# Kernel optimization log

Measured on AMD Instinct MI355X. Metric: run time of the kernel, lower is better.

The kernel has to match this reference:

```python
import jax, jax.numpy as jnp
import numpy as np

B, S, D = 2, 2048, 1024
NH, NKV = 16, 4
HD = D // NH
KVD = NKV * HD
NE, MM = 8, 4
INTER = MM * D // NE  # 512
ROPE_BASE = 10000.0
ALPHA, BETA, GATE, DT = 0.95, 0.3, 0.1, 0.1
MU_MIN, MU_MAX, VMAX = 0.5, 1.5, 3.0


def rms_norm(x):
    # torch F.rms_norm with eps=None -> finfo(dtype).eps, no learned weight
    return x * jax.lax.rsqrt(jnp.mean(x * x, axis=-1, keepdims=True) + jnp.finfo(x.dtype).eps)


def rope_tables(seq_len, dtype):
    inv_freq = 1.0 / ROPE_BASE ** (jnp.arange(0, HD, 2, dtype=jnp.float32) / HD)
    t = jnp.arange(seq_len, dtype=jnp.float32)
    freqs = jnp.outer(t, inv_freq)  # [S, HD/2]
    return jnp.cos(freqs).astype(dtype)[None, None], jnp.sin(freqs).astype(dtype)[None, None]


def apply_rotary(x, cos, sin):
    half = x.shape[-1] // 2
    x1, x2 = x[..., :half], x[..., half:]
    return jnp.concatenate((x1 * cos + x2 * sin, -x1 * sin + x2 * cos), axis=-1)


def attention(n, cq_w, ck_w, cv_w, proj_w, q_gain):
    q = jnp.einsum('bsd,od->bso', n, cq_w).reshape(B, S, NH, HD).transpose(0, 2, 1, 3)
    k = jnp.einsum('bsd,od->bso', n, ck_w).reshape(B, S, NKV, HD).transpose(0, 2, 1, 3)
    v = jnp.einsum('bsd,od->bso', n, cv_w).reshape(B, S, NKV, HD).transpose(0, 2, 1, 3)
    q, k = rms_norm(q), rms_norm(k)
    cos, sin = rope_tables(S, q.dtype)
    q, k = apply_rotary(q, cos, sin), apply_rotary(k, cos, sin)
    q = q * q_gain[None, :, None, None]
    rep = NH // NKV  # GQA: repeat kv heads
    k = jnp.repeat(k, rep, axis=1)
    v = jnp.repeat(v, rep, axis=1)
    scale = 1.0 / np.sqrt(HD).astype(np.float32)
    scores = jnp.einsum('bhqd,bhkd->bhqk', q, k) * scale
    causal = jnp.tril(jnp.ones((S, S), bool))
    scores = jnp.where(causal[None, None], scores, jnp.finfo(scores.dtype).min)
    probs = jax.nn.softmax(scores, axis=-1)
    y = jnp.einsum('bhqk,bhkd->bhqd', probs, v)
    y = y.transpose(0, 2, 1, 3).reshape(B, S, D)
    return jnp.einsum('bsd,od->bso', y, proj_w)


def moe(m, gate_up, down, eids):
    # faithful to TokenRoutedMLP: dense per-expert GEMM, masked accumulate
    flat = m.reshape(-1, D)
    fids = eids.reshape(-1)
    out = jnp.zeros_like(flat)
    for e in range(NE):
        gu = flat @ gate_up[e]                       # [T, 2*INTER]
        g, u = gu[:, :INTER], gu[:, INTER:]
        h = (jax.nn.silu(g) * u) @ down[e]           # [T, D]
        out = out + h * (fids == e)[:, None].astype(flat.dtype)
    return out.reshape(B, S, D)


def setup_inputs():
    key = jax.random.key(0)
    ks = jax.random.split(key, 10)
    w = lambda k, shape: jax.random.normal(k, shape, jnp.float32) * 0.02
    return {
        'x': jax.random.normal(ks[0], (B, S, D), jnp.float32),
        'x0': jax.random.normal(ks[1], (B, S, D), jnp.float32),
        'vel': jnp.zeros((B, S, D), jnp.float32),
        'resid_mix': jnp.stack((jnp.ones(D, jnp.float32), jnp.zeros(D, jnp.float32))),
        'attn_scale': jnp.ones(D, jnp.float32),
        'mlp_scale': jnp.ones(D, jnp.float32),
        'cq_w': w(ks[2], (D, D)),
        'ck_w': w(ks[3], (KVD, D)),
        'cv_w': w(ks[4], (KVD, D)),
        'proj_w': w(ks[5], (D, D)),
        'q_gain': jnp.ones(NH, jnp.float32),
        'mu': jnp.full((D,), 1.0, jnp.float32),
        'gate_up': w(ks[6], (NE, D, 2 * INTER)),
        'down': w(ks[7], (NE, INTER, D)),
        'eids': jax.random.randint(ks[8], (B, S), 0, NE),
    }


def reference(x, x0, vel, resid_mix, attn_scale, mlp_scale, cq_w, ck_w, cv_w, proj_w, q_gain, mu, gate_up, down, eids):
    x = resid_mix[0][None, None, :] * x + resid_mix[1][None, None, :] * x0
    n = rms_norm(x)
    x = x + attn_scale[None, None, :] * attention(n, cq_w, ck_w, cv_w, proj_w, q_gain)
    # PID dynamics
    mu_c = jnp.clip(mu, MU_MIN, MU_MAX)
    v_next = jnp.clip(ALPHA * vel - BETA * (x - mu_c[None, None, :]), -VMAX, VMAX)
    x = x + DT * GATE * v_next
    x = x + mlp_scale[None, None, :] * moe(rms_norm(x), gate_up, down, eids)
    return x, v_next
```

## Files before the change

### kernel.cpp

```cpp
#include <hip/hip_runtime.h>
#include <hip/hip_bf16.h>
#include <math.h>

#define NBATCH 2
#define NSEQ   2048
#define NDIM   1024
#define NHEAD  16
#define NKVH   4
#define HDIM   64
#define KVD    256
#define NEXP   8
#define NINTER 512
#define NTOK   (NBATCH*NSEQ)
#define QKVN   1536
#define MAXTILE 40
#define RMS_EPS 1.1920929e-07f
#define LN_10000 9.210340371976184f
#define QSCALE (0.125f * 1.44269504088896f)
#define DEFER_THR 11.5f

typedef __attribute__((ext_vector_type(8))) short bf16x8;
typedef __attribute__((ext_vector_type(4))) short short4v;
typedef __attribute__((ext_vector_type(4))) float f32x4;

__device__ __forceinline__ short f2b(float f) {
  return __builtin_bit_cast(short, (__bf16)f);
}
__device__ __forceinline__ float b2f(short s) {
  unsigned u = ((unsigned)(unsigned short)s) << 16;
  return __builtin_bit_cast(float, u);
}
__device__ __forceinline__ float ex2(float x) {
  float r; asm("v_exp_f32 %0, %1" : "=v"(r) : "v"(x)); return r;
}
__device__ __forceinline__ void load_lds16(const short* g, short* l) {
  __builtin_amdgcn_global_load_lds((const __attribute__((address_space(1))) void*)g,
                                   (__attribute__((address_space(3))) void*)l, 16, 0, 0);
}

__device__ __forceinline__ float wred64(float v) {
#pragma unroll
  for (int m = 32; m >= 1; m >>= 1) v += __shfl_xor(v, m);
  return v;
}

__global__ __launch_bounds__(256) void k_w_prep(
    const float* __restrict__ cq, const float* __restrict__ ck,
    const float* __restrict__ cv, const float* __restrict__ pw,
    const float* __restrict__ gate_up,
    short* __restrict__ wqkv, short* __restrict__ wproj, short* __restrict__ wgu_t) {
  __shared__ short T[64*66];
  const int bid = blockIdx.x;
  const int t = threadIdx.x;
  if (bid < 2560) {
    const int row = bid;
    const int c = t * 4;
    const float* src; short* dst;
    if (row < 1024)      { src = cq + (size_t)row*NDIM;        dst = wqkv + (size_t)row*NDIM; }
    else if (row < 1280) { src = ck + (size_t)(row-1024)*NDIM; dst = wqkv + (size_t)row*NDIM; }
    else if (row < 1536) { src = cv + (size_t)(row-1280)*NDIM; dst = wqkv + (size_t)row*NDIM; }
    else                 { src = pw + (size_t)(row-1536)*NDIM; dst = wproj + (size_t)(row-1536)*NDIM; }
    float4 v = *(const float4*)(src + c);
    short4v o = {f2b(v.x), f2b(v.y), f2b(v.z), f2b(v.w)};
    *(short4v*)(dst + c) = o;
  } else {
    const int b2 = bid - 2560;
    const int kt = b2 & 15, nt = (b2 >> 4) & 15, e = b2 >> 8;
    const float* ie = gate_up + (size_t)e*1024*1024 + (size_t)(kt*64)*1024 + nt*64;
    short* oe = wgu_t + (size_t)e*1024*1024 + (size_t)(nt*64)*1024 + kt*64;
    const int r = t >> 4, c = (t & 15) * 4;
#pragma unroll
    for (int p = 0; p < 4; ++p) {
      float4 v = *(const float4*)(ie + (size_t)(p*16 + r)*1024 + c);
      T[(p*16 + r)*66 + c + 0] = f2b(v.x);
      T[(p*16 + r)*66 + c + 1] = f2b(v.y);
      T[(p*16 + r)*66 + c + 2] = f2b(v.z);
      T[(p*16 + r)*66 + c + 3] = f2b(v.w);
    }
    __syncthreads();
#pragma unroll
    for (int p = 0; p < 4; ++p) {
      int rr = p*16 + r;
      short4v o = {T[(c+0)*66 + rr], T[(c+1)*66 + rr], T[(c+2)*66 + rr], T[(c+3)*66 + rr]};
      *(short4v*)(oe + (size_t)rr*1024 + c) = o;
    }
  }
}

__global__ __launch_bounds__(256) void k_w_transpose(
    const float* __restrict__ in, short* __restrict__ outp, int KIN, int NIN) {
  __shared__ short T[64*66];
  const int kt = blockIdx.x, nt = blockIdx.y, e = blockIdx.z;
  const float* ie = in + (size_t)e*KIN*NIN + (size_t)(kt*64)*NIN + nt*64;
  short* oe = outp + (size_t)e*NIN*KIN + (size_t)(nt*64)*KIN + kt*64;
  const int t = threadIdx.x;
  const int r = t >> 4, c = (t & 15) * 4;
#pragma unroll
  for (int p = 0; p < 4; ++p) {
    float4 v = *(const float4*)(ie + (size_t)(p*16 + r)*NIN + c);
    T[(p*16 + r)*66 + c + 0] = f2b(v.x);
    T[(p*16 + r)*66 + c + 1] = f2b(v.y);
    T[(p*16 + r)*66 + c + 2] = f2b(v.z);
    T[(p*16 + r)*66 + c + 3] = f2b(v.w);
  }
  __syncthreads();
#pragma unroll
  for (int p = 0; p < 4; ++p) {
    int rr = p*16 + r;
    short4v o = {T[(c+0)*66 + rr], T[(c+1)*66 + rr], T[(c+2)*66 + rr], T[(c+3)*66 + rr]};
    *(short4v*)(oe + (size_t)rr*KIN + c) = o;
  }
}

__global__ __launch_bounds__(256) void k_resid_rms(
    const float* __restrict__ x, const float* __restrict__ x0,
    const float* __restrict__ rmix, short* __restrict__ xr, short* __restrict__ nrm) {
  const int row = blockIdx.x;
  const int t = threadIdx.x;
  const int d = t * 4;
  const size_t base = (size_t)row * NDIM + d;
  float4 a  = *(const float4*)(x  + base);
  float4 b  = *(const float4*)(x0 + base);
  float4 m0 = *(const float4*)(rmix + d);
  float4 m1 = *(const float4*)(rmix + NDIM + d);
  float4 r;
  r.x = m0.x*a.x + m1.x*b.x;
  r.y = m0.y*a.y + m1.y*b.y;
  r.z = m0.z*a.z + m1.z*b.z;
  r.w = m0.w*a.w + m1.w*b.w;
  float ss = r.x*r.x + r.y*r.y + r.z*r.z + r.w*r.w;
  ss = wred64(ss);
  __shared__ float wsum[4];
  if ((t & 63) == 0) wsum[t >> 6] = ss;
  __syncthreads();
  float tot = wsum[0] + wsum[1] + wsum[2] + wsum[3];
  float rms = rsqrtf(tot * (1.0f/NDIM) + RMS_EPS);
  short4v xo = {f2b(r.x), f2b(r.y), f2b(r.z), f2b(r.w)};
  short4v no = {f2b(r.x*rms), f2b(r.y*rms), f2b(r.z*rms), f2b(r.w*rms)};
  *(short4v*)(xr + base) = xo;
  *(short4v*)(nrm + base) = no;
}

template <int MODE>
__global__ __launch_bounds__(256) void k_gemm_mfma(
    const short* __restrict__ A, int lda,
    const short* __restrict__ Bw, int K, int N,
    short* __restrict__ Cb, float* __restrict__ Cf, int ldc,
    const int* __restrict__ rowmap, const int* __restrict__ tiletab,
    const int* __restrict__ meta, const float* __restrict__ mscale) {
  __shared__ short sA[2][128*32];
  __shared__ short sB[2][128*32];
  int row0, end = 0x7fffffff, e = 0;
  if (MODE == 0) {
    row0 = blockIdx.y * 128;
  } else {
    e = tiletab[2*blockIdx.y];
    if (e < 0) return;
    row0 = tiletab[2*blockIdx.y + 1];
    end = meta[1 + e];
  }
  const int t = threadIdx.x;
  const int w = t >> 6, l = t & 63;
  const int wr = (w >> 1) * 64, wc = (w & 1) * 64;
  const int lrow = l & 15, lk8 = (l >> 4) * 8;
  const int srow0 = w*16 + (l >> 2);
  const int scol = (l & 3) * 8;
  const short* Bp = Bw + (size_t)e * N * K + (size_t)(blockIdx.x * 128) * K;
  const short* gA0;
  const short* gA1;
  if (MODE == 1) {
    int s0 = row0 + srow0;      if (s0 >= NTOK) s0 = NTOK - 1;
    int s1 = row0 + 64 + srow0; if (s1 >= NTOK) s1 = NTOK - 1;
    gA0 = A + (size_t)rowmap[s0] * lda + scol;
    gA1 = A + (size_t)rowmap[s1] * lda + scol;
  } else {
    gA0 = A + (size_t)(row0 + srow0) * lda + scol;
    gA1 = A + (size_t)(row0 + 64 + srow0) * lda + scol;
  }
  const short* gB0 = Bp + (size_t)srow0 * K + scol;
  const short* gB1 = Bp + (size_t)(64 + srow0) * K + scol;
  const int lo0 = (w*16)*32;
  const int lo1 = (64 + w*16)*32;
  f32x4 acc[4][4];
#pragma unroll
  for (int m = 0; m < 4; ++m)
#pragma unroll
    for (int n = 0; n < 4; ++n) acc[m][n] = 0.f;
  load_lds16(gA0, sA[0] + lo0);
  load_lds16(gA1, sA[0] + lo1);
  load_lds16(gB0, sB[0] + lo0);
  load_lds16(gB1, sB[0] + lo1);
  gA0 += 32; gA1 += 32; gB0 += 32; gB1 += 32;
  int cur = 0;
  for (int k0 = 0; k0 < K; k0 += 32) {
    __syncthreads();
    if (k0 + 32 < K) {
      load_lds16(gA0, sA[cur^1] + lo0);
      load_lds16(gA1, sA[cur^1] + lo1);
      load_lds16(gB0, sB[cur^1] + lo0);
      load_lds16(gB1, sB[cur^1] + lo1);
      gA0 += 32; gA1 += 32; gB0 += 32; gB1 += 32;
    }
    bf16x8 af[4], bfr[4];
#pragma unroll
    for (int m = 0; m < 4; ++m)
      af[m] = *(const bf16x8*)&sA[cur][(wr + m*16 + lrow)*32 + lk8];
#pragma unroll
    for (int n = 0; n < 4; ++n)
      bfr[n] = *(const bf16x8*)&sB[cur][(wc + n*16 + lrow)*32 + lk8];
    __builtin_amdgcn_s_setprio(1);
#pragma unroll
    for (int m = 0; m < 4; ++m)
#pragma unroll
      for (int n = 0; n < 4; ++n)
        acc[m][n] = __builtin_amdgcn_mfma_f32_16x16x32_bf16(af[m], bfr[n], acc[m][n], 0, 0, 0);
    __builtin_amdgcn_s_setprio(0);
    cur ^= 1;
  }
  const int col0 = blockIdx.x * 128;
  if (MODE <= 1) {
#pragma unroll
    for (int m = 0; m < 4; ++m) {
#pragma unroll
      for (int r = 0; r < 4; ++r) {
        int rr = row0 + wr + m*16 + (l >> 4)*4 + r;
        if (rr < end) {
#pragma unroll
          for (int n = 0; n < 4; ++n)
            Cb[(size_t)rr * ldc + col0 + wc + n*16 + lrow] = f2b(acc[m][n][r]);
        }
      }
    }
  } else {
#pragma unroll
    for (int m = 0; m < 4; ++m) {
#pragma unroll
      for (int r = 0; r < 4; ++r) {
        int slot = row0 + wr + m*16 + (l >> 4)*4 + r;
        if (slot < end) {
          int tok = rowmap[slot];
#pragma unroll
          for (int n = 0; n < 4; ++n) {
            int cc = col0 + wc + n*16 + lrow;
            Cf[(size_t)tok * ldc + cc] += mscale[cc] * acc[m][n][r];
          }
        }
      }
    }
  }
}

__global__ __launch_bounds__(256) void k_qk_norm_rope(
    short* __restrict__ qkv, const float* __restrict__ q_gain) {
  const int row = blockIdx.x;
  const int t = threadIdx.x;
  const int w = t >> 6, lane = t & 63;
  const int s = row & (NSEQ - 1);
  const int fi = lane & 31;
  const float fr = (float)s * expf(-(float)fi * (LN_10000 / 32.0f));
  const float co = cosf(fr), si = sinf(fr);
#pragma unroll
  for (int h = w; h < NHEAD; h += 4) {
    short* p = qkv + (size_t)row*QKVN + h*HDIM + lane;
    float v = b2f(*p);
    float ssum = wred64(v*v);
    float rr = rsqrtf(ssum * (1.0f/HDIM) + RMS_EPS);
    float vn = v * rr;
    float partner = __shfl_xor(vn, 32);
    float o = (lane < 32) ? (vn*co + partner*si) : (vn*co - partner*si);
    *p = f2b(o * q_gain[h] * QSCALE);
  }
  if (w < NKVH) {
    short* p = qkv + (size_t)row*QKVN + 1024 + w*HDIM + lane;
    float v = b2f(*p);
    float ssum = wred64(v*v);
    float rr = rsqrtf(ssum * (1.0f/HDIM) + RMS_EPS);
    float vn = v * rr;
    float partner = __shfl_xor(vn, 32);
    float o = (lane < 32) ? (vn*co + partner*si) : (vn*co - partner*si);
    *p = f2b(o);
  }
}

__global__ __launch_bounds__(256) void k_transpose_v(
    const short* __restrict__ qkv, short* __restrict__ vbT) {
  __shared__ short T[64*72];
  const int blk = blockIdx.x;
  const int st = blk & 31, kh = (blk >> 5) & 3, b = blk >> 7;
  const int t = threadIdx.x;
#pragma unroll
  for (int i = 0; i < 2; ++i) {
    int c = t + i*256;
    int s = c >> 3, d0 = (c & 7) * 8;
    bf16x8 v = *(const bf16x8*)(qkv + (size_t)(b*NSEQ + st*64 + s)*QKVN + 1280 + kh*HDIM + d0);
#pragma unroll
    for (int j = 0; j < 8; ++j) T[(d0 + j)*72 + s] = v[j];
  }
  __syncthreads();
#pragma unroll
  for (int i = 0; i < 2; ++i) {
    int c = t + i*256;
    int d = c >> 3, s0 = (c & 7) * 8;
    *(bf16x8*)(vbT + (size_t)((b*NKVH + kh)*HDIM + d)*NSEQ + st*64 + s0) = *(bf16x8*)&T[d*72 + s0];
  }
}

__global__ __launch_bounds__(256) void k_attn_mfma(
    const short* __restrict__ qkv, const short* __restrict__ vbT, short* __restrict__ y) {
  __shared__ short Ks[2][64*72];
  __shared__ short Vt[2][64*72];
  __shared__ short Ps[64*72];
  const int t = threadIdx.x;
  const int l = t & 63, w = t >> 6;
  const int lrow = l & 15, g = l >> 4, lk8 = g * 8;
  const int bid = blockIdx.x;
  int qt = bid & 15;
  const int h = (bid >> 4) & 15, b = bid >> 8;
  if (b & 1) qt = 15 - qt;
  const int kh = h >> 2;
  bf16x8 qf[2][2];
#pragma unroll
  for (int qra = 0; qra < 2; ++qra) {
    int qrow_g = b*NSEQ + qt*128 + qra*64 + w*16 + lrow;
#pragma unroll
    for (int hf = 0; hf < 2; ++hf)
      qf[qra][hf] = *(const bf16x8*)(qkv + (size_t)qrow_g*QKVN + h*HDIM + hf*32 + lk8);
  }
  const int r0a = t >> 3;
  const int d0a = (t & 7) * 8;
  const short* kgbase = qkv + 1024 + (size_t)kh*HDIM;
  const short* vgbase = vbT + (size_t)((b*NKVH + kh)*HDIM)*NSEQ;
  bf16x8 kr0, kr1, vr0, vr1;
#define LOADKV(KT) do { \
    kr0 = *(const bf16x8*)(kgbase + (size_t)(b*NSEQ + (KT)*64 + r0a)*QKVN + d0a); \
    kr1 = *(const bf16x8*)(kgbase + (size_t)(b*NSEQ + (KT)*64 + r0a + 32)*QKVN + d0a); \
    vr0 = *(const bf16x8*)(vgbase + (size_t)r0a*NSEQ + (KT)*64 + d0a); \
    vr1 = *(const bf16x8*)(vgbase + (size_t)(r0a + 32)*NSEQ + (KT)*64 + d0a); \
  } while (0)
  float m_i[2] = {-INFINITY, -INFINITY};
  float l_i[2] = {0.f, 0.f};
  f32x4 O[2][4];
#pragma unroll
  for (int qra = 0; qra < 2; ++qra)
#pragma unroll
    for (int db = 0; db < 4; ++db) O[qra][db] = 0.f;
  const int ktmax = 2*qt + 1;
  LOADKV(0);
  for (int kt = 0; kt <= ktmax; ++kt) {
    const int buf = kt & 1;
    *(bf16x8*)&Ks[buf][r0a*72 + d0a] = kr0;
    *(bf16x8*)&Ks[buf][(r0a + 32)*72 + d0a] = kr1;
    *(bf16x8*)&Vt[buf][r0a*72 + d0a] = vr0;
    *(bf16x8*)&Vt[buf][(r0a + 32)*72 + d0a] = vr1;
    __syncthreads();
    if (kt < ktmax) LOADKV(kt + 1);
    bf16x8 kf[4][2];
#pragma unroll
    for (int nb = 0; nb < 4; ++nb) {
      kf[nb][0] = *(const bf16x8*)&Ks[buf][(nb*16 + lrow)*72 + lk8];
      kf[nb][1] = *(const bf16x8*)&Ks[buf][(nb*16 + lrow)*72 + 32 + lk8];
    }
    const int qra0 = (kt == ktmax) ? 1 : 0;
    bf16x8 pf[2][2];
#pragma unroll
    for (int qra = 0; qra < 2; ++qra) {
      if (qra >= qra0) {
        f32x4 sc[4];
#pragma unroll
        for (int nb = 0; nb < 4; ++nb) sc[nb] = 0.f;
        __builtin_amdgcn_s_setprio(1);
#pragma unroll
        for (int nb = 0; nb < 4; ++nb) {
          sc[nb] = __builtin_amdgcn_mfma_f32_16x16x32_bf16(kf[nb][0], qf[qra][0], sc[nb], 0, 0, 0);
          sc[nb] = __builtin_amdgcn_mfma_f32_16x16x32_bf16(kf[nb][1], qf[qra][1], sc[nb], 0, 0, 0);
        }
        __builtin_amdgcn_s_setprio(0);
        if (kt >= 2*qt) {
          int qg = qt*128 + qra*64 + w*16 + lrow;
#pragma unroll
          for (int nb = 0; nb < 4; ++nb)
#pragma unroll
            for (int r = 0; r < 4; ++r)
              if (kt*64 + nb*16 + g*4 + r > qg) sc[nb][r] = -INFINITY;
        }
        float rm = sc[0][0];
#pragma unroll
        for (int nb = 0; nb < 4; ++nb)
#pragma unroll
          for (int r = 0; r < 4; ++r) rm = fmaxf(rm, sc[nb][r]);
        rm = fmaxf(rm, __shfl_xor(rm, 16));
        rm = fmaxf(rm, __shfl_xor(rm, 32));
        if (!__all(rm <= m_i[qra] + DEFER_THR)) {
          float mn = fmaxf(m_i[qra], rm);
          float fac = ex2(m_i[qra] - mn);
          l_i[qra] *= fac;
          m_i[qra] = mn;
#pragma unroll
          for (int r = 0; r < 4; ++r) {
            float ff = __shfl(fac, g*4 + r);
#pragma unroll
            for (int db = 0; db < 4; ++db) O[qra][db][r] *= ff;
          }
        }
        float rs = 0.f;
#pragma unroll
        for (int nb = 0; nb < 4; ++nb) {
#pragma unroll
          for (int r = 0; r < 4; ++r) {
            float p = ex2(sc[nb][r] - m_i[qra]);
            sc[nb][r] = p;
            rs += p;
          }
        }
        rs += __shfl_xor(rs, 16);
        rs += __shfl_xor(rs, 32);
        l_i[qra] += rs;
        short* prow = &Ps[(w*16 + lrow)*72];
#pragma unroll
        for (int nb = 0; nb < 4; ++nb) {
          short4v pk = {f2b(sc[nb][0]), f2b(sc[nb][1]), f2b(sc[nb][2]), f2b(sc[nb][3])};
          *(short4v*)(prow + nb*16 + g*4) = pk;
        }
        pf[qra][0] = *(const bf16x8*)&Ps[(w*16 + lrow)*72 + lk8];
        pf[qra][1] = *(const bf16x8*)&Ps[(w*16 + lrow)*72 + 32 + lk8];
      }
    }
    __builtin_amdgcn_s_setprio(1);
#pragma unroll
    for (int db = 0; db < 4; ++db) {
      bf16x8 vf0 = *(const bf16x8*)&Vt[buf][(db*16 + lrow)*72 + lk8];
      bf16x8 vf1 = *(const bf16x8*)&Vt[buf][(db*16 + lrow)*72 + 32 + lk8];
      if (qra0 == 0) {
        O[0][db] = __builtin_amdgcn_mfma_f32_16x16x32_bf16(pf[0][0], vf0, O[0][db], 0, 0, 0);
        O[0][db] = __builtin_amdgcn_mfma_f32_16x16x32_bf16(pf[0][1], vf1, O[0][db], 0, 0, 0);
      }
      O[1][db] = __builtin_amdgcn_mfma_f32_16x16x32_bf16(pf[1][0], vf0, O[1][db], 0, 0, 0);
      O[1][db] = __builtin_amdgcn_mfma_f32_16x16x32_bf16(pf[1][1], vf1, O[1][db], 0, 0, 0);
    }
    __builtin_amdgcn_s_setprio(0);
  }
#undef LOADKV
#pragma unroll
  for (int qra = 0; qra < 2; ++qra) {
    float linv = 1.0f / l_i[qra];
#pragma unroll
    for (int r = 0; r < 4; ++r) {
      float inv = __shfl(linv, g*4 + r);
      int rowo = b*NSEQ + qt*128 + qra*64 + w*16 + g*4 + r;
#pragma unroll
      for (int db = 0; db < 4; ++db)
        y[(size_t)rowo*NDIM + h*HDIM + db*16 + lrow] = f2b(O[qra][db][r] * inv);
    }
  }
}

__global__ __launch_bounds__(256) void k_fuse_vel(
    const short* __restrict__ xr, const short* __restrict__ aout,
    const float* __restrict__ vel, const float* __restrict__ ascale,
    const float* __restrict__ mu, float* __restrict__ out, short* __restrict__ mbuf) {
  const int row = blockIdx.x;
  const int t = threadIdx.x;
  const int d = t * 4;
  const size_t base = (size_t)row * NDIM + d;
  short4v a4 = *(const short4v*)(xr + base);
  short4v o4 = *(const short4v*)(aout + base);
  float4 vv = *(const float4*)(vel + base);
  float4 as = *(const float4*)(ascale + d);
  float4 mu4 = *(const float4*)(mu + d);
  float xs[4], vns[4];
  const float asl[4] = {as.x, as.y, as.z, as.w};
  const float mul[4] = {mu4.x, mu4.y, mu4.z, mu4.w};
  const float vvl[4] = {vv.x, vv.y, vv.z, vv.w};
#pragma unroll
  for (int i = 0; i < 4; ++i) {
    float x1 = b2f(a4[i]) + asl[i] * b2f(o4[i]);
    float muc = fminf(fmaxf(mul[i], 0.5f), 1.5f);
    float vn = fminf(fmaxf(0.95f*vvl[i] - 0.3f*(x1 - muc), -3.f), 3.f);
    xs[i] = x1 + 0.01f*vn;
    vns[i] = vn;
  }
  float4 x2 = {xs[0], xs[1], xs[2], xs[3]};
  float4 vnq = {vns[0], vns[1], vns[2], vns[3]};
  *(float4*)(out + base) = x2;
  *(float4*)(out + (size_t)NTOK*NDIM + base) = vnq;
  float ss = xs[0]*xs[0] + xs[1]*xs[1] + xs[2]*xs[2] + xs[3]*xs[3];
  ss = wred64(ss);
  __shared__ float wsum[4];
  if ((t & 63) == 0) wsum[t >> 6] = ss;
  __syncthreads();
  float tot = wsum[0] + wsum[1] + wsum[2] + wsum[3];
  float rms = rsqrtf(tot * (1.0f/NDIM) + RMS_EPS);
  short4v m4 = {f2b(xs[0]*rms), f2b(xs[1]*rms), f2b(xs[2]*rms), f2b(xs[3]*rms)};
  *(short4v*)(mbuf + base) = m4;
}

__global__ __launch_bounds__(256) void k_route(
    const int* __restrict__ eids, int* __restrict__ rowmap,
    int* __restrict__ tiletab, int* __restrict__ meta) {
  __shared__ int cnt[NEXP];
  __shared__ int ctr[NEXP];
  const int t = threadIdx.x;
  if (t < NEXP) cnt[t] = 0;
  __syncthreads();
  for (int i = t; i < NTOK; i += 256) atomicAdd(&cnt[eids[i]], 1);
  __syncthreads();
  if (t == 0) {
    int off = 0, tile = 0;
    for (int e = 0; e < NEXP; ++e) {
      ctr[e] = off;
      int nt_e = (cnt[e] + 127) >> 7;
      for (int j = 0; j < nt_e; ++j) { tiletab[2*tile] = e; tiletab[2*tile+1] = off + j*128; ++tile; }
      off += cnt[e];
      meta[1 + e] = off;
    }
    meta[0] = tile;
    for (int j = tile; j < MAXTILE; ++j) { tiletab[2*j] = -1; tiletab[2*j+1] = 0; }
  }
  __syncthreads();
  for (int i = t; i < NTOK; i += 256) {
    int e = eids[i];
    int slot = atomicAdd(&ctr[e], 1);
    rowmap[slot] = i;
  }
}

__global__ __launch_bounds__(256) void k_silu(
    const short* __restrict__ gu, short* __restrict__ hb) {
  int gid = blockIdx.x * 256 + threadIdx.x;
  int row = gid >> 7, c4 = (gid & 127) * 4;
  short4v g = *(const short4v*)(gu + (size_t)row*1024 + c4);
  short4v u = *(const short4v*)(gu + (size_t)row*1024 + 512 + c4);
  short4v o;
#pragma unroll
  for (int i = 0; i < 4; ++i) {
    float gf = b2f(g[i]), uf = b2f(u[i]);
    o[i] = f2b(gf / (1.0f + __expf(-gf)) * uf);
  }
  *(short4v*)(hb + (size_t)row*512 + c4) = o;
}

extern "C" void kernel_launch(void* const* d_in, const int* in_sizes, int n_in,
                              void* d_out, int out_size, void* d_ws, size_t ws_size,
                              hipStream_t stream) {
  const float* x      = (const float*)d_in[0];
  const float* x0     = (const float*)d_in[1];
  const float* vel    = (const float*)d_in[2];
  const float* rmix   = (const float*)d_in[3];
  const float* ascale = (const float*)d_in[4];
  const float* mscale = (const float*)d_in[5];
  const float* cq_w   = (const float*)d_in[6];
  const float* ck_w   = (const float*)d_in[7];
  const float* cv_w   = (const float*)d_in[8];
  const float* proj_w = (const float*)d_in[9];
  const float* q_gain = (const float*)d_in[10];
  const float* mu     = (const float*)d_in[11];
  const float* gate_up= (const float*)d_in[12];
  const float* down   = (const float*)d_in[13];
  const int*   eids   = (const int*)d_in[14];
  float* out = (float*)d_out;
  char* base = (char*)d_ws;

  const size_t MB = 1024*1024;
  short* wqkv  = (short*)base;
  short* wproj = (short*)(base + 3*MB);
  int*   rowmap  = (int*)(base + 5*MB);
  int*   tiletab = rowmap + NTOK;
  int*   meta    = tiletab + 2*MAXTILE;
  short* wgu_t = (short*)(base + 6*MB);
  short* hbuf  = wgu_t;
  short* xr    = (short*)(base + 22*MB);
  short* gu    = xr;
  short* nbuf  = (short*)(base + 30*MB);
  short* ybuf  = nbuf;
  short* mbuf  = nbuf;
  short* wdn_t = nbuf;
  short* qkv   = (short*)(base + 38*MB);
  short* aout  = qkv;
  short* vbT   = (short*)(base + 50*MB);

  k_w_prep<<<4608, 256, 0, stream>>>(cq_w, ck_w, cv_w, proj_w, gate_up, wqkv, wproj, wgu_t);
  k_resid_rms<<<NTOK, 256, 0, stream>>>(x, x0, rmix, xr, nbuf);
  k_gemm_mfma<0><<<dim3(QKVN/128, NTOK/128), 256, 0, stream>>>(
      nbuf, NDIM, wqkv, NDIM, QKVN, qkv, nullptr, QKVN, nullptr, nullptr, nullptr, nullptr);
  k_qk_norm_rope<<<NTOK, 256, 0, stream>>>(qkv, q_gain);
  k_transpose_v<<<NBATCH*NKVH*(NSEQ/64), 256, 0, stream>>>(qkv, vbT);
  k_attn_mfma<<<NBATCH*NHEAD*(NSEQ/128), 256, 0, stream>>>(qkv, vbT, ybuf);
  k_gemm_mfma<0><<<dim3(NDIM/128, NTOK/128), 256, 0, stream>>>(
      ybuf, NDIM, wproj, NDIM, NDIM, aout, nullptr, NDIM, nullptr, nullptr, nullptr, nullptr);
  k_fuse_vel<<<NTOK, 256, 0, stream>>>(xr, aout, vel, ascale, mu, out, mbuf);
  k_route<<<1, 256, 0, stream>>>(eids, rowmap, tiletab, meta);
  k_gemm_mfma<1><<<dim3(1024/128, MAXTILE), 256, 0, stream>>>(
      mbuf, NDIM, wgu_t, NDIM, 1024, gu, nullptr, 1024, rowmap, tiletab, meta, nullptr);
  k_w_transpose<<<dim3(8, 16, 8), 256, 0, stream>>>(down, wdn_t, 512, 1024);
  k_silu<<<(NTOK*512)/(4*256), 256, 0, stream>>>(gu, hbuf);
  k_gemm_mfma<2><<<dim3(NDIM/128, MAXTILE), 256, 0, stream>>>(
      hbuf, NINTER, wdn_t, NINTER, NDIM, nullptr, out, NDIM, rowmap, tiletab, meta, mscale);
}
```

Measured before the change: 227.0 us.

## Fuse SiLU into gate-up GEMM epilogue and V transpose into rope kernel

The gate_up weights are stored with gate and up rows interleaved in 16-row groups, so each GEMM tile holds matching gate and up columns and can apply SiLU(g)*u in its epilogue. This removes the separate SiLU kernel and the round trip of the full gate/up intermediate through memory. The V transpose is also folded into the q/k norm+rope kernel, with its first blocks doing the transpose, which drops one launch. In exchange, the GEMM epilogue does more math and the rope kernel carries shared memory plus extra work in some blocks.

Result: faster. 221.7 us (-2.4%).

```diff
diff --git a/kernel.cpp b/kernel.cpp
--- a/kernel.cpp
+++ b/kernel.cpp
@@ -18,6 +18,7 @@
 #define LN_10000 9.210340371976184f
 #define QSCALE (0.125f * 1.44269504088896f)
 #define DEFER_THR 11.5f
+#define LOG2E 1.44269504088896f
 
 typedef __attribute__((ext_vector_type(8))) short bf16x8;
 typedef __attribute__((ext_vector_type(4))) short short4v;
@@ -67,7 +68,7 @@
     const int b2 = bid - 2560;
     const int kt = b2 & 15, nt = (b2 >> 4) & 15, e = b2 >> 8;
     const float* ie = gate_up + (size_t)e*1024*1024 + (size_t)(kt*64)*1024 + nt*64;
-    short* oe = wgu_t + (size_t)e*1024*1024 + (size_t)(nt*64)*1024 + kt*64;
+    short* we = wgu_t + (size_t)e*1024*1024;
     const int r = t >> 4, c = (t & 15) * 4;
 #pragma unroll
     for (int p = 0; p < 4; ++p) {
@@ -81,8 +82,11 @@
 #pragma unroll
     for (int p = 0; p < 4; ++p) {
       int rr = p*16 + r;
+      int R = nt*64 + rr;
+      int Rn = (R < 512) ? ((R & ~15)*2 + (R & 15))
+                         : (((R - 512) & ~15)*2 + 16 + (R & 15));
       short4v o = {T[(c+0)*66 + rr], T[(c+1)*66 + rr], T[(c+2)*66 + rr], T[(c+3)*66 + rr]};
-      *(short4v*)(oe + (size_t)rr*1024 + c) = o;
+      *(short4v*)(we + (size_t)Rn*1024 + kt*64 + c) = o;
     }
   }
 }
@@ -168,7 +172,7 @@
   const short* Bp = Bw + (size_t)e * N * K + (size_t)(blockIdx.x * 128) * K;
   const short* gA0;
   const short* gA1;
-  if (MODE == 1) {
+  if (MODE == 1 || MODE == 3) {
     int s0 = row0 + srow0;      if (s0 >= NTOK) s0 = NTOK - 1;
     int s1 = row0 + 64 + srow0; if (s1 >= NTOK) s1 = NTOK - 1;
     gA0 = A + (size_t)rowmap[s0] * lda + scol;
@@ -231,7 +235,7 @@
         }
       }
     }
-  } else {
+  } else if (MODE == 2) {
 #pragma unroll
     for (int m = 0; m < 4; ++m) {
 #pragma unroll
@@ -247,11 +251,29 @@
         }
       }
     }
+  } else {
+    const int fbBase = (col0 + wc) >> 5;
+#pragma unroll
+    for (int m = 0; m < 4; ++m) {
+#pragma unroll
+      for (int r = 0; r < 4; ++r) {
+        int slot = row0 + wr + m*16 + (l >> 4)*4 + r;
+        if (slot < end) {
+#pragma unroll
+          for (int p = 0; p < 2; ++p) {
+            float gg = acc[m][2*p][r], uu = acc[m][2*p+1][r];
+            float sg = 1.0f / (1.0f + ex2(-LOG2E * gg));
+            Cb[(size_t)slot * NINTER + (fbBase + p)*16 + lrow] = f2b(gg * sg * uu);
+          }
+        }
+      }
+    }
   }
 }
 
 __global__ __launch_bounds__(256) void k_qk_norm_rope(
-    short* __restrict__ qkv, const float* __restrict__ q_gain) {
+    short* __restrict__ qkv, const float* __restrict__ q_gain, short* __restrict__ vbT) {
+  __shared__ short T[64*72];
   const int row = blockIdx.x;
   const int t = threadIdx.x;
   const int w = t >> 6, lane = t & 63;
@@ -280,28 +302,23 @@
     float o = (lane < 32) ? (vn*co + partner*si) : (vn*co - partner*si);
     *p = f2b(o);
   }
-}
-
-__global__ __launch_bounds__(256) void k_transpose_v(
-    const short* __restrict__ qkv, short* __restrict__ vbT) {
-  __shared__ short T[64*72];
-  const int blk = blockIdx.x;
-  const int st = blk & 31, kh = (blk >> 5) & 3, b = blk >> 7;
-  const int t = threadIdx.x;
-#pragma unroll
-  for (int i = 0; i < 2; ++i) {
-    int c = t + i*256;
-    int s = c >> 3, d0 = (c & 7) * 8;
-    bf16x8 v = *(const bf16x8*)(qkv + (size_t)(b*NSEQ + st*64 + s)*QKVN + 1280 + kh*HDIM + d0);
-#pragma unroll
-    for (int j = 0; j < 8; ++j) T[(d0 + j)*72 + s] = v[j];
-  }
-  __syncthreads();
-#pragma unroll
-  for (int i = 0; i < 2; ++i) {
-    int c = t + i*256;
-    int d = c >> 3, s0 = (c & 7) * 8;
-    *(bf16x8*)(vbT + (size_t)((b*NKVH + kh)*HDIM + d)*NSEQ + st*64 + s0) = *(bf16x8*)&T[d*72 + s0];
+  if (row < 256) {
+    const int st = row & 31, kh = (row >> 5) & 3, b = row >> 7;
+#pragma unroll
+    for (int i = 0; i < 2; ++i) {
+      int c = t + i*256;
+      int sV = c >> 3, d0 = (c & 7) * 8;
+      bf16x8 v = *(const bf16x8*)(qkv + (size_t)(b*NSEQ + st*64 + sV)*QKVN + 1280 + kh*HDIM + d0);
+#pragma unroll
+      for (int j = 0; j < 8; ++j) T[(d0 + j)*72 + sV] = v[j];
+    }
+    __syncthreads();
+#pragma unroll
+    for (int i = 0; i < 2; ++i) {
+      int c = t + i*256;
+      int d = c >> 3, s0 = (c & 7) * 8;
+      *(bf16x8*)(vbT + (size_t)((b*NKVH + kh)*HDIM + d)*NSEQ + st*64 + s0) = *(bf16x8*)&T[d*72 + s0];
+    }
   }
 }
 
@@ -522,21 +539,6 @@
     int slot = atomicAdd(&ctr[e], 1);
     rowmap[slot] = i;
   }
-}
-
-__global__ __launch_bounds__(256) void k_silu(
-    const short* __restrict__ gu, short* __restrict__ hb) {
-  int gid = blockIdx.x * 256 + threadIdx.x;
-  int row = gid >> 7, c4 = (gid & 127) * 4;
-  short4v g = *(const short4v*)(gu + (size_t)row*1024 + c4);
-  short4v u = *(const short4v*)(gu + (size_t)row*1024 + 512 + c4);
-  short4v o;
-#pragma unroll
-  for (int i = 0; i < 4; ++i) {
-    float gf = b2f(g[i]), uf = b2f(u[i]);
-    o[i] = f2b(gf / (1.0f + __expf(-gf)) * uf);
-  }
-  *(short4v*)(hb + (size_t)row*512 + c4) = o;
 }
 
 extern "C" void kernel_launch(void* const* d_in, const int* in_sizes, int n_in,
@@ -567,9 +569,8 @@
   int*   tiletab = rowmap + NTOK;
   int*   meta    = tiletab + 2*MAXTILE;
   short* wgu_t = (short*)(base + 6*MB);
-  short* hbuf  = wgu_t;
   short* xr    = (short*)(base + 22*MB);
-  short* gu    = xr;
+  short* hbuf  = xr;
   short* nbuf  = (short*)(base + 30*MB);
   short* ybuf  = nbuf;
   short* mbuf  = nbuf;
@@ -582,17 +583,15 @@
   k_resid_rms<<<NTOK, 256, 0, stream>>>(x, x0, rmix, xr, nbuf);
   k_gemm_mfma<0><<<dim3(QKVN/128, NTOK/128), 256, 0, stream>>>(
       nbuf, NDIM, wqkv, NDIM, QKVN, qkv, nullptr, QKVN, nullptr, nullptr, nullptr, nullptr);
-  k_qk_norm_rope<<<NTOK, 256, 0, stream>>>(qkv, q_gain);
-  k_transpose_v<<<NBATCH*NKVH*(NSEQ/64), 256, 0, stream>>>(qkv, vbT);
+  k_qk_norm_rope<<<NTOK, 256, 0, stream>>>(qkv, q_gain, vbT);
   k_attn_mfma<<<NBATCH*NHEAD*(NSEQ/128), 256, 0, stream>>>(qkv, vbT, ybuf);
   k_gemm_mfma<0><<<dim3(NDIM/128, NTOK/128), 256, 0, stream>>>(
       ybuf, NDIM, wproj, NDIM, NDIM, aout, nullptr, NDIM, nullptr, nullptr, nullptr, nullptr);
   k_fuse_vel<<<NTOK, 256, 0, stream>>>(xr, aout, vel, ascale, mu, out, mbuf);
   k_route<<<1, 256, 0, stream>>>(eids, rowmap, tiletab, meta);
-  k_gemm_mfma<1><<<dim3(1024/128, MAXTILE), 256, 0, stream>>>(
-      mbuf, NDIM, wgu_t, NDIM, 1024, gu, nullptr, 1024, rowmap, tiletab, meta, nullptr);
+  k_gemm_mfma<3><<<dim3(1024/128, MAXTILE), 256, 0, stream>>>(
+      mbuf, NDIM, wgu_t, NDIM, 1024, hbuf, nullptr, NINTER, rowmap, tiletab, meta, nullptr);
   k_w_transpose<<<dim3(8, 16, 8), 256, 0, stream>>>(down, wdn_t, 512, 1024);
-  k_silu<<<(NTOK*512)/(4*256), 256, 0, stream>>>(gu, hbuf);
   k_gemm_mfma<2><<<dim3(NDIM/128, MAXTILE), 256, 0, stream>>>(
       hbuf, NINTER, wdn_t, NINTER, NDIM, nullptr, out, NDIM, rowmap, tiletab, meta, mscale);
 }
```
